# Optimization experiments

Measured on AMD Instinct MI355X. Metric: run time of the kernel, lower is better.

The kernel has to match this reference:

```python
import jax, jax.numpy as jnp
import numpy as np

# Faithful emulation of SQBnBLinear: SmoothQuant rescale fused with
# bnb Linear8bitLt (threshold=0.0 => no fp16 outlier path):
#   w_sq = weight / scales ; x_sq = x * scales
#   row-wise absmax int8 quantization of both x (per token) and w (per out row)
#   int8 GEMM, then dequant with (ax * aw / 127^2), plus bias / scales.

B, S, D = 4, 2048, 4096

def setup_inputs() -> dict:
    key = jax.random.key(0)
    k1, k2, k3, k4 = jax.random.split(key, 4)
    x = jax.random.normal(k1, (B, S, D), dtype=jnp.float32)
    weight = jax.random.normal(k2, (D, D), dtype=jnp.float32) * 0.02
    bias = jax.random.normal(k3, (D,), dtype=jnp.float32) * 0.02
    # SmoothQuant scales are positive per-input-channel factors
    scales = jax.random.uniform(k4, (D,), dtype=jnp.float32, minval=0.5, maxval=2.0)
    return {"x": x, "weight": weight, "bias": bias, "scales": scales}

def _quantize_rowwise(t):
    # symmetric per-row (last-dim) absmax int8 quantization
    absmax = jnp.max(jnp.abs(t), axis=-1, keepdims=True)
    absmax = jnp.maximum(absmax, 1e-8)
    q = jnp.clip(jnp.round(t * (127.0 / absmax)), -127.0, 127.0)
    return q, absmax

def reference(x, weight, bias, scales):
    # __init__: fold SmoothQuant scales into weight and bias
    w_sq = weight / scales            # [out, in] / [in]
    b_sq = bias / scales              # valid because in_features == out_features
    # forward: rescale input (mul_ by scales)
    x_sq = x * scales                 # [B, S, in]
    # LLM.int8() with threshold=0.0: pure int8 path
    qx, ax = _quantize_rowwise(x_sq)  # qx [B,S,in], ax [B,S,1]
    qw, aw = _quantize_rowwise(w_sq)  # qw [out,in], aw [out,1]
    acc = jnp.einsum('bsi,oi->bso', qx, qw)  # int accumulate (emulated in fp32)
    out = acc * (ax / 127.0) * (aw[:, 0] / 127.0) + b_sq
    return out
```

## Files before the change

### kernel.cpp

```cpp
#include <hip/hip_runtime.h>
#include <stdint.h>

#define DDIM 4096
#define MTOK 8192

typedef __attribute__((ext_vector_type(4))) int i32x4;
typedef __attribute__((ext_vector_type(16))) int i32x16;

__device__ __forceinline__ void async16(const void* g, void* l) {
    __builtin_amdgcn_global_load_lds(
        (const __attribute__((address_space(1))) unsigned int*)g,
        (__attribute__((address_space(3))) unsigned int*)l,
        16, 0, 0);
}

__global__ __launch_bounds__(256) void quant_all(
    const float* __restrict__ x, const float* __restrict__ weight,
    const float* __restrict__ scales,
    signed char* __restrict__ qx, float* __restrict__ sx,
    signed char* __restrict__ qw, float* __restrict__ sw,
    const float* __restrict__ bias, float* __restrict__ bq)
{
    __shared__ float red[4];
    const int tid = threadIdx.x;
    const bool is_x = blockIdx.x < MTOK;
    const int row = is_x ? blockIdx.x : (blockIdx.x - MTOK);
    const float* src = is_x ? (x + (size_t)row * DDIM) : (weight + (size_t)row * DDIM);
    signed char* q = is_x ? qx : qw;
    float* srow = is_x ? sx : sw;

    const float4* s4 = (const float4*)scales;
    const float4* x4 = (const float4*)src;

    float4 v[4];
    float am = 0.0f;
#pragma unroll
    for (int j = 0; j < 4; ++j) {
        float4 a = x4[tid + j * 256];
        float4 s = s4[tid + j * 256];
        float4 r;
        if (is_x) { r.x = a.x * s.x; r.y = a.y * s.y; r.z = a.z * s.z; r.w = a.w * s.w; }
        else      { r.x = a.x / s.x; r.y = a.y / s.y; r.z = a.z / s.z; r.w = a.w / s.w; }
        v[j] = r;
        am = fmaxf(am, fmaxf(fmaxf(fabsf(r.x), fabsf(r.y)),
                             fmaxf(fabsf(r.z), fabsf(r.w))));
    }
#pragma unroll
    for (int off = 32; off > 0; off >>= 1)
        am = fmaxf(am, __shfl_xor(am, off, 64));
    if ((tid & 63) == 0) red[tid >> 6] = am;
    __syncthreads();
    am = fmaxf(fmaxf(red[0], red[1]), fmaxf(red[2], red[3]));
    am = fmaxf(am, 1e-8f);

    const float sc = 127.0f / am;
    uint32_t* qrow = (uint32_t*)(q + (size_t)row * DDIM);
#pragma unroll
    for (int j = 0; j < 4; ++j) {
        int q0 = (int)fminf(127.0f, fmaxf(-127.0f, rintf(v[j].x * sc)));
        int q1 = (int)fminf(127.0f, fmaxf(-127.0f, rintf(v[j].y * sc)));
        int q2 = (int)fminf(127.0f, fmaxf(-127.0f, rintf(v[j].z * sc)));
        int q3 = (int)fminf(127.0f, fmaxf(-127.0f, rintf(v[j].w * sc)));
        qrow[tid + j * 256] = (uint32_t)(q0 & 0xff) | ((uint32_t)(q1 & 0xff) << 8) |
                              ((uint32_t)(q2 & 0xff) << 16) | ((uint32_t)(q3 & 0xff) << 24);
    }
    if (tid == 0) {
        srow[row] = am * (1.0f / 127.0f);
        if (!is_x) bq[row] = bias[row] / scales[row];
    }
}

__global__ __launch_bounds__(256) void gemm_i8(
    const signed char* __restrict__ qx, const signed char* __restrict__ qw,
    const float* __restrict__ sx, const float* __restrict__ sw,
    const float* __restrict__ bq, float* __restrict__ out)
{
    __shared__ __align__(16) signed char sA[128 * 128];
    __shared__ __align__(16) signed char sB[128 * 128];

    const int K = DDIM, N = DDIM;
    const int tid  = threadIdx.x;
    const int bm   = blockIdx.y;
    const int bn   = blockIdx.x;
    const int wave = tid >> 6;
    const int lane = tid & 63;
    const int wm   = (wave & 1) << 6;
    const int wn   = (wave >> 1) << 6;
    const int r5   = lane & 31;
    const int hi   = lane >> 5;

    const signed char* Ab = qx + (size_t)bm * 128 * K;
    const signed char* Bb = qw + (size_t)bn * 128 * K;

    const int srow0 = tid >> 3;
    const int cir   = tid & 7;

    int roff[4];
#pragma unroll
    for (int kq = 0; kq < 4; ++kq)
        roff[kq] = (((kq * 2 + hi) ^ (r5 & 7)) << 4);

    i32x16 acc[2][2] = {};

    for (int k0 = 0; k0 < K; k0 += 128) {
#pragma unroll
        for (int c = 0; c < 4; ++c) {
            const int row = srow0 + 32 * c;
            const int kc  = cir ^ (row & 7);
            const int p   = tid * 16 + c * 4096;
            async16(Ab + (size_t)row * K + k0 + kc * 16, &sA[p]);
            async16(Bb + (size_t)row * K + k0 + kc * 16, &sB[p]);
        }
        __syncthreads();

#pragma unroll
        for (int kq = 0; kq < 4; ++kq) {
            i32x4 a0 = *(const i32x4*)&sA[(wm +      r5) * 128 + roff[kq]];
            i32x4 a1 = *(const i32x4*)&sA[(wm + 32 + r5) * 128 + roff[kq]];
            i32x4 b0 = *(const i32x4*)&sB[(wn +      r5) * 128 + roff[kq]];
            i32x4 b1 = *(const i32x4*)&sB[(wn + 32 + r5) * 128 + roff[kq]];
            acc[0][0] = __builtin_amdgcn_mfma_i32_32x32x32_i8(a0, b0, acc[0][0], 0, 0, 0);
            acc[0][1] = __builtin_amdgcn_mfma_i32_32x32x32_i8(a0, b1, acc[0][1], 0, 0, 0);
            acc[1][0] = __builtin_amdgcn_mfma_i32_32x32x32_i8(a1, b0, acc[1][0], 0, 0, 0);
            acc[1][1] = __builtin_amdgcn_mfma_i32_32x32x32_i8(a1, b1, acc[1][1], 0, 0, 0);
        }

        __syncthreads();
    }

#pragma unroll
    for (int mi = 0; mi < 2; ++mi) {
#pragma unroll
        for (int nj = 0; nj < 2; ++nj) {
            const int n = bn * 128 + wn + nj * 32 + r5;
            const float swn = sw[n];
            const float bqn = bq[n];
            const int mbase = bm * 128 + wm + mi * 32 + 4 * hi;
#pragma unroll
            for (int r = 0; r < 16; ++r) {
                const int m = mbase + (r & 3) + 8 * (r >> 2);
                out[(size_t)m * N + n] = (float)acc[mi][nj][r] * sx[m] * swn + bqn;
            }
        }
    }
}

extern "C" void kernel_launch(void* const* d_in, const int* in_sizes, int n_in,
                              void* d_out, int out_size, void* d_ws, size_t ws_size,
                              hipStream_t stream) {
    const float* x      = (const float*)d_in[0];
    const float* weight = (const float*)d_in[1];
    const float* bias   = (const float*)d_in[2];
    const float* scales = (const float*)d_in[3];
    float* out = (float*)d_out;

    char* ws = (char*)d_ws;
    signed char* qx = (signed char*)ws;
    signed char* qw = (signed char*)(ws + 33554432);
    float* sx = (float*)(ws + 50331648);
    float* sw = (float*)(ws + 50364416);
    float* bq = (float*)(ws + 50380800);

    quant_all<<<MTOK + DDIM, 256, 0, stream>>>(x, weight, scales, qx, sx, qw, sw, bias, bq);

    dim3 grid(DDIM / 128, MTOK / 128);
    gemm_i8<<<grid, 256, 0, stream>>>(qx, qw, sx, sw, bq, out);
}
```

Measured before the change: 418.0 us.

## Enlarge int8 GEMM tiles to 256x256 with double-buffered async LDS loads

Grows the GEMM block tile from 128x128 to 256x256 with 512 threads, so each wave now computes a 128x64 sub-tile with 8 MFMA accumulators. It double-buffers the LDS tiles and prefetches the next K-tile with global_load_lds, waiting on vmcnt instead of doing a full sync. Together these aim to overlap global-to-LDS traffic with the MFMAs and raise operand reuse per byte loaded. It also adds per-step barriers and s_setprio around the MFMA bursts, and hoists the sx loads out of the epilogue loop. The cost is 128KB of LDS per block, which allows only one block per CU, and a grid of just 512 blocks.

Result: no change. 422.9 us (+1.2%).

```diff
diff --git a/kernel.cpp b/kernel.cpp
--- a/kernel.cpp
+++ b/kernel.cpp
@@ -3,6 +3,7 @@
 
 #define DDIM 4096
 #define MTOK 8192
+#define KTILES (DDIM / 128)
 
 typedef __attribute__((ext_vector_type(4))) int i32x4;
 typedef __attribute__((ext_vector_type(16))) int i32x16;
@@ -70,13 +71,13 @@
     }
 }
 
-__global__ __launch_bounds__(256) void gemm_i8(
+__global__ __launch_bounds__(512, 2) void gemm_i8(
     const signed char* __restrict__ qx, const signed char* __restrict__ qw,
     const float* __restrict__ sx, const float* __restrict__ sw,
     const float* __restrict__ bq, float* __restrict__ out)
 {
-    __shared__ __align__(16) signed char sA[128 * 128];
-    __shared__ __align__(16) signed char sB[128 * 128];
+    __shared__ __align__(16) signed char sA[2][256 * 128];
+    __shared__ __align__(16) signed char sB[2][256 * 128];
 
     const int K = DDIM, N = DDIM;
     const int tid  = threadIdx.x;
@@ -84,62 +85,98 @@
     const int bn   = blockIdx.x;
     const int wave = tid >> 6;
     const int lane = tid & 63;
-    const int wm   = (wave & 1) << 6;
-    const int wn   = (wave >> 1) << 6;
+    const int wm   = (wave >> 2) << 7;
+    const int wn   = (wave & 3) << 6;
     const int r5   = lane & 31;
     const int hi   = lane >> 5;
 
-    const signed char* Ab = qx + (size_t)bm * 128 * K;
-    const signed char* Bb = qw + (size_t)bn * 128 * K;
-
-    const int srow0 = tid >> 3;
-    const int cir   = tid & 7;
+    const signed char* Ab = qx + (size_t)bm * 256 * K;
+    const signed char* Bb = qw + (size_t)bn * 256 * K;
+
+    const int srow = tid >> 3;
+    const int cir  = tid & 7;
 
     int roff[4];
 #pragma unroll
     for (int kq = 0; kq < 4; ++kq)
         roff[kq] = (((kq * 2 + hi) ^ (r5 & 7)) << 4);
 
-    i32x16 acc[2][2] = {};
-
-    for (int k0 = 0; k0 < K; k0 += 128) {
-#pragma unroll
-        for (int c = 0; c < 4; ++c) {
-            const int row = srow0 + 32 * c;
-            const int kc  = cir ^ (row & 7);
-            const int p   = tid * 16 + c * 4096;
-            async16(Ab + (size_t)row * K + k0 + kc * 16, &sA[p]);
-            async16(Bb + (size_t)row * K + k0 + kc * 16, &sB[p]);
+    i32x16 acc[4][2] = {};
+
+#pragma unroll
+    for (int c = 0; c < 4; ++c) {
+        const int row = srow + 64 * c;
+        const int kc  = cir ^ (row & 7);
+        const int p   = tid * 16 + c * 8192;
+        async16(Ab + (size_t)row * K + kc * 16, &sA[0][p]);
+        async16(Bb + (size_t)row * K + kc * 16, &sB[0][p]);
+    }
+
+    for (int kt = 0; kt < KTILES; ++kt) {
+        const int cur = kt & 1;
+
+        if (kt + 1 < KTILES) {
+            const int k0n = (kt + 1) * 128;
+#pragma unroll
+            for (int c = 0; c < 4; ++c) {
+                const int row = srow + 64 * c;
+                const int kc  = cir ^ (row & 7);
+                const int p   = tid * 16 + c * 8192;
+                async16(Ab + (size_t)row * K + k0n + kc * 16, &sA[cur ^ 1][p]);
+                async16(Bb + (size_t)row * K + k0n + kc * 16, &sB[cur ^ 1][p]);
+            }
+            asm volatile("s_waitcnt vmcnt(8)" ::: "memory");
+        } else {
+            asm volatile("s_waitcnt vmcnt(0)" ::: "memory");
         }
-        __syncthreads();
-
-#pragma unroll
-        for (int kq = 0; kq < 4; ++kq) {
-            i32x4 a0 = *(const i32x4*)&sA[(wm +      r5) * 128 + roff[kq]];
-            i32x4 a1 = *(const i32x4*)&sA[(wm + 32 + r5) * 128 + roff[kq]];
-            i32x4 b0 = *(const i32x4*)&sB[(wn +      r5) * 128 + roff[kq]];
-            i32x4 b1 = *(const i32x4*)&sB[(wn + 32 + r5) * 128 + roff[kq]];
+        __builtin_amdgcn_s_barrier();
+        __builtin_amdgcn_sched_barrier(0);
+
+        const signed char* sAc = sA[cur];
+        const signed char* sBc = sB[cur];
+
+#pragma unroll
+        for (int p = 0; p < 4; ++p) {
+            i32x4 a0 = *(const i32x4*)&sAc[(wm +      r5) * 128 + roff[p]];
+            i32x4 a1 = *(const i32x4*)&sAc[(wm + 32 + r5) * 128 + roff[p]];
+            i32x4 a2 = *(const i32x4*)&sAc[(wm + 64 + r5) * 128 + roff[p]];
+            i32x4 a3 = *(const i32x4*)&sAc[(wm + 96 + r5) * 128 + roff[p]];
+            i32x4 b0 = *(const i32x4*)&sBc[(wn +      r5) * 128 + roff[p]];
+            i32x4 b1 = *(const i32x4*)&sBc[(wn + 32 + r5) * 128 + roff[p]];
+
+            __builtin_amdgcn_s_barrier();
+
+            __builtin_amdgcn_s_setprio(1);
             acc[0][0] = __builtin_amdgcn_mfma_i32_32x32x32_i8(a0, b0, acc[0][0], 0, 0, 0);
             acc[0][1] = __builtin_amdgcn_mfma_i32_32x32x32_i8(a0, b1, acc[0][1], 0, 0, 0);
             acc[1][0] = __builtin_amdgcn_mfma_i32_32x32x32_i8(a1, b0, acc[1][0], 0, 0, 0);
             acc[1][1] = __builtin_amdgcn_mfma_i32_32x32x32_i8(a1, b1, acc[1][1], 0, 0, 0);
+            acc[2][0] = __builtin_amdgcn_mfma_i32_32x32x32_i8(a2, b0, acc[2][0], 0, 0, 0);
+            acc[2][1] = __builtin_amdgcn_mfma_i32_32x32x32_i8(a2, b1, acc[2][1], 0, 0, 0);
+            acc[3][0] = __builtin_amdgcn_mfma_i32_32x32x32_i8(a3, b0, acc[3][0], 0, 0, 0);
+            acc[3][1] = __builtin_amdgcn_mfma_i32_32x32x32_i8(a3, b1, acc[3][1], 0, 0, 0);
+            __builtin_amdgcn_s_setprio(0);
+
+            if (p < 3) __builtin_amdgcn_s_barrier();
         }
-
-        __syncthreads();
-    }
-
-#pragma unroll
-    for (int mi = 0; mi < 2; ++mi) {
+    }
+
+#pragma unroll
+    for (int mi = 0; mi < 4; ++mi) {
+        const int mbase = bm * 256 + wm + mi * 32 + 4 * hi;
+        float sxv[16];
+#pragma unroll
+        for (int r = 0; r < 16; ++r)
+            sxv[r] = sx[mbase + (r & 3) + 8 * (r >> 2)];
 #pragma unroll
         for (int nj = 0; nj < 2; ++nj) {
-            const int n = bn * 128 + wn + nj * 32 + r5;
+            const int n = bn * 256 + wn + nj * 32 + r5;
             const float swn = sw[n];
             const float bqn = bq[n];
-            const int mbase = bm * 128 + wm + mi * 32 + 4 * hi;
 #pragma unroll
             for (int r = 0; r < 16; ++r) {
                 const int m = mbase + (r & 3) + 8 * (r >> 2);
-                out[(size_t)m * N + n] = (float)acc[mi][nj][r] * sx[m] * swn + bqn;
+                out[(size_t)m * N + n] = (float)acc[mi][nj][r] * sxv[r] * swn + bqn;
             }
         }
     }
@@ -163,6 +200,6 @@
 
     quant_all<<<MTOK + DDIM, 256, 0, stream>>>(x, weight, scales, qx, sx, qw, sw, bias, bq);
 
-    dim3 grid(DDIM / 128, MTOK / 128);
-    gemm_i8<<<grid, 256, 0, stream>>>(qx, qw, sx, sw, bq, out);
-}
+    dim3 grid(DDIM / 256, MTOK / 256);
+    gemm_i8<<<grid, 512, 0, stream>>>(qx, qw, sx, sw, bq, out);
+}
```
